# Optimization experiments

Measured on AMD Instinct MI355X. Metric: run time of the kernel, lower is better.

## Reference

```python
import jax, jax.numpy as jnp
import numpy as np

N_ATOMS = 100000
N_EDGES = 300000
ATOM_DIM = 32
BOND_DIM = 16
STEPS = 4


def setup_inputs() -> dict:
    key = jax.random.key(0)
    ks = jax.random.split(key, 8)
    atom_features = jax.random.normal(ks[0], (N_ATOMS, ATOM_DIM), dtype=jnp.float32)
    bond_features = jax.random.normal(ks[1], (N_EDGES, BOND_DIM), dtype=jnp.float32)
    pair_indices = jax.random.randint(ks[2], (N_EDGES, 2), 0, N_ATOMS, dtype=jnp.int64 if jax.config.jax_enable_x64 else jnp.int32)
    W_bond = jax.random.normal(ks[3], (BOND_DIM, ATOM_DIM * ATOM_DIM), dtype=jnp.float32) * 0.05
    b_bond = jnp.zeros((ATOM_DIM * ATOM_DIM,), dtype=jnp.float32)
    W_ih = jax.random.normal(ks[4], (3 * ATOM_DIM, ATOM_DIM), dtype=jnp.float32) * 0.1
    W_hh = jax.random.normal(ks[5], (3 * ATOM_DIM, ATOM_DIM), dtype=jnp.float32) * 0.1
    b_ih = jnp.zeros((3 * ATOM_DIM,), dtype=jnp.float32)
    b_hh = jnp.zeros((3 * ATOM_DIM,), dtype=jnp.float32)
    return {
        'atom_features': atom_features,
        'bond_features': bond_features,
        'pair_indices': pair_indices,
        'W_bond': W_bond, 'b_bond': b_bond,
        'W_ih': W_ih, 'W_hh': W_hh, 'b_ih': b_ih, 'b_hh': b_hh,
    }


def _gru_cell(x, h, W_ih, W_hh, b_ih, b_hh):
    # torch.nn.GRUCell semantics
    gi = x @ W_ih.T + b_ih  # [N, 3H]
    gh = h @ W_hh.T + b_hh
    i_r, i_z, i_n = jnp.split(gi, 3, axis=-1)
    h_r, h_z, h_n = jnp.split(gh, 3, axis=-1)
    r = jax.nn.sigmoid(i_r + h_r)
    z = jax.nn.sigmoid(i_z + h_z)
    n = jnp.tanh(i_n + r * h_n)
    return (1.0 - z) * n + z * h


def reference(atom_features, bond_features, pair_indices, W_bond, b_bond, W_ih, W_hh, b_ih, b_hh):
    n_atoms, d = atom_features.shape
    # Edge transform matrices (identical every step in the original; hoisted)
    edge_mats = (bond_features @ W_bond + b_bond).reshape(-1, d, d)  # [E, d, d]
    dst = pair_indices[:, 0]
    nbr = pair_indices[:, 1]
    h = atom_features
    for _ in range(STEPS):
        # gather neighbor states, per-edge matvec, scatter-add
        msg = jnp.einsum('eij,ej->ei', edge_mats, h[nbr])  # [E, d]
        agg = jax.ops.segment_sum(msg, dst, num_segments=n_atoms)  # [N, d]
        h = _gru_cell(agg, h, W_ih, W_hh, b_ih, b_hh)
    return h
```

## Files before the change

kernel.cpp:

```cpp
#include <hip/hip_runtime.h>

#define NA 100000
#define NE 300000
#define STEPS 4
#define NTILES (NE / 16)
#define ATILES (NA / 16)

typedef _Float16 f16;
typedef _Float16 half8 __attribute__((ext_vector_type(8)));
typedef _Float16 half4 __attribute__((ext_vector_type(4)));
using f32x4 = __attribute__((ext_vector_type(4))) float;

__global__ __launch_bounds__(256) void zero_kernel(float4* __restrict__ p, int n4)
{
    int t = blockIdx.x * 256 + threadIdx.x;
    if (t < n4) p[t] = make_float4(0.f, 0.f, 0.f, 0.f);
}

__global__ __launch_bounds__(256) void conv_kernel(
    const float* __restrict__ src, f16* __restrict__ dst, int n8)
{
    int t = blockIdx.x * 256 + threadIdx.x;
    if (t >= n8) return;
    float4 a = reinterpret_cast<const float4*>(src)[2 * t];
    float4 b = reinterpret_cast<const float4*>(src)[2 * t + 1];
    half8 o;
    o[0]=(f16)a.x; o[1]=(f16)a.y; o[2]=(f16)a.z; o[3]=(f16)a.w;
    o[4]=(f16)b.x; o[5]=(f16)b.y; o[6]=(f16)b.z; o[7]=(f16)b.w;
    reinterpret_cast<half8*>(dst)[t] = o;
}

__global__ __launch_bounds__(256) void prep_kernel(
    const float* __restrict__ Wb, const float* __restrict__ bb,
    const float* __restrict__ Wih, const float* __restrict__ Whh,
    f16* __restrict__ Wbt, f16* __restrict__ Wihb, f16* __restrict__ Whhb)
{
    int t = blockIdx.x * 256 + threadIdx.x;
    if (t < 17 * 32 * 32) {
        int j = t & 31, i = (t >> 5) & 31, k = t >> 10;
        float v = (k < 16) ? Wb[k * 1024 + i * 32 + j] : bb[i * 32 + j];
        Wbt[t] = (f16)v;
    } else if (t < 17 * 32 * 32 + 3072) {
        int u = t - 17 * 32 * 32;
        Wihb[u] = (f16)Wih[u];
    } else if (t < 17 * 32 * 32 + 6144) {
        int u = t - 17 * 32 * 32 - 3072;
        Whhb[u] = (f16)Whh[u];
    }
}

__global__ __launch_bounds__(256) void hist_kernel(
    const int* __restrict__ pair, int* __restrict__ cnt)
{
    int e = blockIdx.x * 256 + threadIdx.x;
    if (e < NE) atomicAdd(&cnt[reinterpret_cast<const int2*>(pair)[e].x], 1);
}

__global__ __launch_bounds__(1024) void scan1_kernel(
    const int* __restrict__ cnt, int* __restrict__ excl, int* __restrict__ bsum)
{
    __shared__ int tmp[1024];
    int g = blockIdx.x * 1024 + threadIdx.x;
    int v = (g < NA) ? cnt[g] : 0;
    tmp[threadIdx.x] = v;
    __syncthreads();
    for (int off = 1; off < 1024; off <<= 1) {
        int u = (threadIdx.x >= off) ? tmp[threadIdx.x - off] : 0;
        __syncthreads();
        tmp[threadIdx.x] += u;
        __syncthreads();
    }
    if (g < NA) excl[g] = tmp[threadIdx.x] - v;
    if (threadIdx.x == 1023) bsum[blockIdx.x] = tmp[1023];
}

__global__ __launch_bounds__(128) void scan2_kernel(int* __restrict__ bsum, int nb)
{
    __shared__ int tmp[128];
    int i = threadIdx.x;
    int v = (i < nb) ? bsum[i] : 0;
    tmp[i] = v;
    __syncthreads();
    for (int off = 1; off < 128; off <<= 1) {
        int u = (i >= off) ? tmp[i - off] : 0;
        __syncthreads();
        tmp[i] += u;
        __syncthreads();
    }
    if (i < nb) bsum[i] = tmp[i] - v;
}

__global__ __launch_bounds__(256) void scan3_kernel(
    const int* __restrict__ excl, const int* __restrict__ bsum,
    int* __restrict__ rowptr, int* __restrict__ next)
{
    int g = blockIdx.x * 256 + threadIdx.x;
    if (g < NA) {
        int v = excl[g] + bsum[g >> 10];
        rowptr[g] = v;
        next[g] = v;
    }
    if (g == NA) rowptr[NA] = NE;
}

__global__ __launch_bounds__(256) void scatter_kernel(
    const float* __restrict__ bond, const int* __restrict__ pair,
    int* __restrict__ next, int* __restrict__ nbrp, f16* __restrict__ bondp)
{
    int e = blockIdx.x * 256 + threadIdx.x;
    if (e >= NE) return;
    int2 p = reinterpret_cast<const int2*>(pair)[e];
    int pos = atomicAdd(&next[p.x], 1);
    nbrp[pos] = p.y;
    const float4* b4 = reinterpret_cast<const float4*>(bond + (size_t)e * 16);
    float4 b0 = b4[0], b1 = b4[1], b2 = b4[2], b3 = b4[3];
    half8 o0, o1;
    o0[0]=(f16)b0.x; o0[1]=(f16)b0.y; o0[2]=(f16)b0.z; o0[3]=(f16)b0.w;
    o0[4]=(f16)b1.x; o0[5]=(f16)b1.y; o0[6]=(f16)b1.z; o0[7]=(f16)b1.w;
    o1[0]=(f16)b2.x; o1[1]=(f16)b2.y; o1[2]=(f16)b2.z; o1[3]=(f16)b2.w;
    o1[4]=(f16)b3.x; o1[5]=(f16)b3.y; o1[6]=(f16)b3.z; o1[7]=(f16)b3.w;
    half8* dst = reinterpret_cast<half8*>(bondp + (size_t)pos * 16);
    dst[0] = o0; dst[1] = o1;
}

__global__ __launch_bounds__(256, 2) void msg_kernel(
    const f16* __restrict__ hb,
    const f16* __restrict__ bondp,
    const int* __restrict__ nbrp,
    const f16* __restrict__ Wbt,
    f16* __restrict__ msg)
{
    int wave = threadIdx.x >> 6;
    int lane = threadIdx.x & 63;
    int col  = lane & 15;
    int kg   = lane >> 4;

    half8 w0[17], w1[17];
#pragma unroll
    for (int s = 0; s < 17; ++s) {
        w0[s] = *reinterpret_cast<const half8*>(Wbt + (s * 32 + col) * 32 + kg * 8);
        w1[s] = *reinterpret_cast<const half8*>(Wbt + (s * 32 + 16 + col) * 32 + kg * 8);
    }

    int wid = blockIdx.x * 4 + wave;
    int nw  = gridDim.x << 2;

    for (int tile = wid; tile < NTILES; tile += nw) {
        int pos = tile * 16 + col;
        int nbr = nbrp[pos];
        half8 hf = *reinterpret_cast<const half8*>(hb + (size_t)nbr * 32 + kg * 8);
        half8 cA = *reinterpret_cast<const half8*>(bondp + (size_t)pos * 16);
        half8 cB = *reinterpret_cast<const half8*>(bondp + (size_t)pos * 16 + 8);

        f32x4 acc0 = {0.f, 0.f, 0.f, 0.f};
        f32x4 acc1 = {0.f, 0.f, 0.f, 0.f};
#pragma unroll
        for (int s = 0; s < 16; ++s) {
            f16 ch = (s < 8) ? cA[s] : cB[s - 8];
            half8 a = hf * ch;
            acc0 = __builtin_amdgcn_mfma_f32_16x16x32_f16(w0[s], a, acc0, 0, 0, 0);
            acc1 = __builtin_amdgcn_mfma_f32_16x16x32_f16(w1[s], a, acc1, 0, 0, 0);
        }
        acc0 = __builtin_amdgcn_mfma_f32_16x16x32_f16(w0[16], hf, acc0, 0, 0, 0);
        acc1 = __builtin_amdgcn_mfma_f32_16x16x32_f16(w1[16], hf, acc1, 0, 0, 0);

        half4 s0, s1;
        s0[0]=(f16)acc0[0]; s0[1]=(f16)acc0[1]; s0[2]=(f16)acc0[2]; s0[3]=(f16)acc0[3];
        s1[0]=(f16)acc1[0]; s1[1]=(f16)acc1[1]; s1[2]=(f16)acc1[2]; s1[3]=(f16)acc1[3];
        *reinterpret_cast<half4*>(msg + (size_t)pos * 32 + kg * 4)      = s0;
        *reinterpret_cast<half4*>(msg + (size_t)pos * 32 + 16 + kg * 4) = s1;
    }
}

__global__ __launch_bounds__(256) void gru_kernel(
    const f16* __restrict__ msg,
    const int* __restrict__ rowptr,
    const f16* __restrict__ hb,
    const f16* __restrict__ Wihb,
    const f16* __restrict__ Whhb,
    const float* __restrict__ bih, const float* __restrict__ bhh,
    float* __restrict__ hout, f16* __restrict__ hbf, int write_f32)
{
    int wave = threadIdx.x >> 6;
    int lane = threadIdx.x & 63;
    int tile = blockIdx.x * 4 + wave;
    if (tile >= ATILES) return;

    int base = tile * 16;
    int col  = lane & 15;
    int kg   = lane >> 4;
    int a0   = base + col;

    float xs[8] = {0.f, 0.f, 0.f, 0.f, 0.f, 0.f, 0.f, 0.f};
    int st = rowptr[a0], en = rowptr[a0 + 1];
    for (int p = st; p < en; ++p) {
        half8 m = *reinterpret_cast<const half8*>(msg + (size_t)p * 32 + kg * 8);
#pragma unroll
        for (int j = 0; j < 8; ++j) xs[j] += (float)m[j];
    }
    half8 xfrag;
#pragma unroll
    for (int j = 0; j < 8; ++j) xfrag[j] = (f16)xs[j];

    half8 hfrag = *reinterpret_cast<const half8*>(hb + (size_t)a0 * 32 + kg * 8);

    f32x4 gi[6], gh[6];
#pragma unroll
    for (int t = 0; t < 6; ++t) {
        half8 bi = *reinterpret_cast<const half8*>(Wihb + (size_t)(t * 16 + col) * 32 + kg * 8);
        half8 bh = *reinterpret_cast<const half8*>(Whhb + (size_t)(t * 16 + col) * 32 + kg * 8);
        f32x4 z = {0.f, 0.f, 0.f, 0.f};
        gi[t] = __builtin_amdgcn_mfma_f32_16x16x32_f16(xfrag, bi, z, 0, 0, 0);
        gh[t] = __builtin_amdgcn_mfma_f32_16x16x32_f16(hfrag, bh, z, 0, 0, 0);
    }

#pragma unroll
    for (int hh = 0; hh < 2; ++hh) {
        int i  = hh * 16 + col;
        float br  = bih[i]      + bhh[i];
        float bz  = bih[32 + i] + bhh[32 + i];
        float bin = bih[64 + i];
        float bhn = bhh[64 + i];
#pragma unroll
        for (int reg = 0; reg < 4; ++reg) {
            int a = base + kg * 4 + reg;
            float r = 1.f / (1.f + __expf(-(gi[hh][reg] + gh[hh][reg] + br)));
            float z = 1.f / (1.f + __expf(-(gi[2 + hh][reg] + gh[2 + hh][reg] + bz)));
            float n = tanhf(gi[4 + hh][reg] + bin + r * (gh[4 + hh][reg] + bhn));
            float hp = (float)hb[(size_t)a * 32 + i];
            float o  = (1.f - z) * n + z * hp;
            if (write_f32) hout[(size_t)a * 32 + i] = o;
            hbf[(size_t)a * 32 + i] = (f16)o;
        }
    }
}

extern "C" void kernel_launch(void* const* d_in, const int* in_sizes, int n_in,
                              void* d_out, int out_size, void* d_ws, size_t ws_size,
                              hipStream_t stream)
{
    const float* atom = (const float*)d_in[0];
    const float* bond = (const float*)d_in[1];
    const int*   pair = (const int*)  d_in[2];
    const float* Wb   = (const float*)d_in[3];
    const float* bb   = (const float*)d_in[4];
    const float* W_ih = (const float*)d_in[5];
    const float* W_hh = (const float*)d_in[6];
    const float* b_ih = (const float*)d_in[7];
    const float* b_hh = (const float*)d_in[8];
    float* out = (float*)d_out;

    char* w = (char*)d_ws;
    f16* msg    = (f16*)w;
    f16* hbf    = (f16*)(w + 19200000);
    f16* bondp  = (f16*)(w + 25600000);
    f16* Wbt    = (f16*)(w + 35200000);
    f16* Wihb   = Wbt + 17 * 32 * 32;
    f16* Whhb   = Wihb + 96 * 32;
    int* rowcnt = (int*)(w + 35248000);
    int* excl   = (int*)(w + 35648000);
    int* bsum   = (int*)(w + 36048000);
    int* rowptr = (int*)(w + 36048512);
    int* next   = (int*)(w + 36448516);
    int* nbrp   = (int*)(w + 36848516);

    const int nsb = (NA + 1023) / 1024;

    zero_kernel<<<(NA * 4 / 16 + 255) / 256, 256, 0, stream>>>((float4*)rowcnt, NA * 4 / 16);
    hist_kernel<<<(NE + 255) / 256, 256, 0, stream>>>(pair, rowcnt);
    scan1_kernel<<<nsb, 1024, 0, stream>>>(rowcnt, excl, bsum);
    scan2_kernel<<<1, 128, 0, stream>>>(bsum, nsb);
    scan3_kernel<<<(NA + 1 + 255) / 256, 256, 0, stream>>>(excl, bsum, rowptr, next);
    scatter_kernel<<<(NE + 255) / 256, 256, 0, stream>>>(bond, pair, next, nbrp, bondp);

    prep_kernel<<<(17 * 32 * 32 + 6144 + 255) / 256, 256, 0, stream>>>(
        Wb, bb, W_ih, W_hh, Wbt, Wihb, Whhb);
    conv_kernel<<<(NA * 32 / 8 + 255) / 256, 256, 0, stream>>>(atom, hbf, NA * 32 / 8);

    const int gru_blocks = (ATILES + 3) / 4;
    for (int s = 0; s < STEPS; ++s) {
        msg_kernel<<<512, 256, 0, stream>>>(hbf, bondp, nbrp, Wbt, msg);
        gru_kernel<<<gru_blocks, 256, 0, stream>>>(msg, rowptr, hbf, Wihb, Whhb,
                                                   b_ih, b_hh, out, hbf,
                                                   (s == STEPS - 1) ? 1 : 0);
    }
}
```

Measured before the change: 209.9 us.

## Prefetch next edge tile, permute bond weights for 16-byte message stores, unroll gather

```diff
diff --git a/kernel.cpp b/kernel.cpp
--- a/kernel.cpp
+++ b/kernel.cpp
@@ -8,7 +8,6 @@
 
 typedef _Float16 f16;
 typedef _Float16 half8 __attribute__((ext_vector_type(8)));
-typedef _Float16 half4 __attribute__((ext_vector_type(4)));
 using f32x4 = __attribute__((ext_vector_type(4))) float;
 
 __global__ __launch_bounds__(256) void zero_kernel(float4* __restrict__ p, int n4)
@@ -39,7 +38,8 @@
     if (t < 17 * 32 * 32) {
         int j = t & 31, i = (t >> 5) & 31, k = t >> 10;
         float v = (k < 16) ? Wb[k * 1024 + i * 32 + j] : bb[i * 32 + j];
-        Wbt[t] = (f16)v;
+        int row = ((i & 4) ? 16 : 0) + ((i >> 3) << 2) + (i & 3);
+        Wbt[(k * 32 + row) * 32 + j] = (f16)v;
     } else if (t < 17 * 32 * 32 + 3072) {
         int u = t - 17 * 32 * 32;
         Wihb[u] = (f16)Wih[u];
@@ -145,12 +145,28 @@
     int wid = blockIdx.x * 4 + wave;
     int nw  = gridDim.x << 2;
 
-    for (int tile = wid; tile < NTILES; tile += nw) {
-        int pos = tile * 16 + col;
+    int tile = wid;
+    int pos = 0;
+    half8 hf{}, cA{}, cB{};
+    if (tile < NTILES) {
+        pos = tile * 16 + col;
         int nbr = nbrp[pos];
-        half8 hf = *reinterpret_cast<const half8*>(hb + (size_t)nbr * 32 + kg * 8);
-        half8 cA = *reinterpret_cast<const half8*>(bondp + (size_t)pos * 16);
-        half8 cB = *reinterpret_cast<const half8*>(bondp + (size_t)pos * 16 + 8);
+        cA = *reinterpret_cast<const half8*>(bondp + (size_t)pos * 16);
+        cB = *reinterpret_cast<const half8*>(bondp + (size_t)pos * 16 + 8);
+        hf = *reinterpret_cast<const half8*>(hb + (size_t)nbr * 32 + kg * 8);
+    }
+
+    while (tile < NTILES) {
+        int tile2 = tile + nw;
+        int pos2 = 0;
+        half8 hf2{}, cA2{}, cB2{};
+        if (tile2 < NTILES) {
+            pos2 = tile2 * 16 + col;
+            int nbr2 = nbrp[pos2];
+            cA2 = *reinterpret_cast<const half8*>(bondp + (size_t)pos2 * 16);
+            cB2 = *reinterpret_cast<const half8*>(bondp + (size_t)pos2 * 16 + 8);
+            hf2 = *reinterpret_cast<const half8*>(hb + (size_t)nbr2 * 32 + kg * 8);
+        }
 
         f32x4 acc0 = {0.f, 0.f, 0.f, 0.f};
         f32x4 acc1 = {0.f, 0.f, 0.f, 0.f};
@@ -164,11 +180,12 @@
         acc0 = __builtin_amdgcn_mfma_f32_16x16x32_f16(w0[16], hf, acc0, 0, 0, 0);
         acc1 = __builtin_amdgcn_mfma_f32_16x16x32_f16(w1[16], hf, acc1, 0, 0, 0);
 
-        half4 s0, s1;
-        s0[0]=(f16)acc0[0]; s0[1]=(f16)acc0[1]; s0[2]=(f16)acc0[2]; s0[3]=(f16)acc0[3];
-        s1[0]=(f16)acc1[0]; s1[1]=(f16)acc1[1]; s1[2]=(f16)acc1[2]; s1[3]=(f16)acc1[3];
-        *reinterpret_cast<half4*>(msg + (size_t)pos * 32 + kg * 4)      = s0;
-        *reinterpret_cast<half4*>(msg + (size_t)pos * 32 + 16 + kg * 4) = s1;
+        half8 so;
+        so[0]=(f16)acc0[0]; so[1]=(f16)acc0[1]; so[2]=(f16)acc0[2]; so[3]=(f16)acc0[3];
+        so[4]=(f16)acc1[0]; so[5]=(f16)acc1[1]; so[6]=(f16)acc1[2]; so[7]=(f16)acc1[3];
+        *reinterpret_cast<half8*>(msg + (size_t)pos * 32 + kg * 8) = so;
+
+        tile = tile2; pos = pos2; hf = hf2; cA = cA2; cB = cB2;
     }
 }
 
@@ -193,7 +210,14 @@
 
     float xs[8] = {0.f, 0.f, 0.f, 0.f, 0.f, 0.f, 0.f, 0.f};
     int st = rowptr[a0], en = rowptr[a0 + 1];
-    for (int p = st; p < en; ++p) {
+    int p = st;
+    for (; p + 1 < en; p += 2) {
+        half8 m0 = *reinterpret_cast<const half8*>(msg + (size_t)p * 32 + kg * 8);
+        half8 m1 = *reinterpret_cast<const half8*>(msg + (size_t)(p + 1) * 32 + kg * 8);
+#pragma unroll
+        for (int j = 0; j < 8; ++j) xs[j] += (float)m0[j] + (float)m1[j];
+    }
+    if (p < en) {
         half8 m = *reinterpret_cast<const half8*>(msg + (size_t)p * 32 + kg * 8);
 #pragma unroll
         for (int j = 0; j < 8; ++j) xs[j] += (float)m[j];
```

Measured after the change: 200.4 us. 1.05x faster.
